# Optimization experiments

Hardware: AMD Instinct MI355X
Metric: run time of the kernel (lower is better)

The kernel has to match this reference:

```python
import jax, jax.numpy as jnp
import numpy as np

B, C, H, W = 4, 16, 512, 512


def setup_inputs() -> dict:
    key = jax.random.key(0)
    k1, k2, k3, k4, k5 = jax.random.split(key, 5)
    # positive depth in [0.5, 10.5] meters
    depth = jax.random.uniform(k1, (B, 1, H, W), dtype=jnp.float32) * 10.0 + 0.5
    # realistic, well-conditioned camera intrinsics per batch element
    fx = 500.0 + 20.0 * jax.random.normal(k2, (B,), dtype=jnp.float32)
    fy = 500.0 + 20.0 * jax.random.normal(k3, (B,), dtype=jnp.float32)
    zeros = jnp.zeros((B,), jnp.float32)
    ones = jnp.ones((B,), jnp.float32)
    K = jnp.stack([
        jnp.stack([fx, zeros, ones * (W / 2.0)], axis=-1),
        jnp.stack([zeros, fy, ones * (H / 2.0)], axis=-1),
        jnp.stack([zeros, zeros, ones], axis=-1),
    ], axis=1)  # [B,3,3]
    # near-identity rigid-ish transforms so homogeneous w ~ 1
    T = jnp.eye(4, dtype=jnp.float32)[None, None] + 0.05 * jax.random.normal(k4, (B, C, 4, 4), dtype=jnp.float32)
    masks = jax.random.randint(k5, (B, C, H, W), 0, 2).astype(jnp.bool_)
    return {"depth": depth, "K": K, "T": T, "masks": masks}


def reference(depth, K, T, masks):
    b, _, h, w = depth.shape
    c = masks.shape[1]
    n = h * w
    eps = 1e-10
    # --- depth -> point cloud ---
    u = jnp.arange(w, dtype=depth.dtype)
    v = jnp.arange(h, dtype=depth.dtype)
    uu, vv = jnp.meshgrid(u, v, indexing='xy')            # [H,W]
    uv1 = jnp.stack([uu, vv, jnp.ones_like(uu)], axis=-1)  # [H,W,3]
    K_inv = jnp.linalg.inv(K)                              # [B,3,3]
    d = jnp.transpose(depth, (0, 2, 3, 1))                 # [B,H,W,1]
    points_3d = jnp.einsum('bij,hwj->bhwi', K_inv, uv1) * d  # [B,H,W,3]
    # --- per-object masked transform (vectorized over all channels) ---
    pts = points_3d.reshape(b, n, 3)
    pts_h = jnp.concatenate([pts, jnp.ones((b, n, 1), pts.dtype)], axis=-1)  # [B,N,4]
    trans_h = jnp.einsum('bcij,bnj->bcni', T, pts_h)       # [B,C,N,4]
    trans3 = trans_h[..., :3] / (trans_h[..., 3:] + eps)   # [B,C,N,3]
    masks_flat = masks.reshape(b, c, n)
    out = pts
    for ci in range(c):
        out = jnp.where(masks_flat[:, ci, :, None], trans3[:, ci], out)
    tp = out.reshape(b, h, w, 3)                           # transformed points
    # --- reproject to depth map (scatter) ---
    p2h = jnp.einsum('bij,bhwj->bhwi', K, tp)              # [B,H,W,3]
    p2 = p2h[..., :2] / (p2h[..., 2:] + eps)
    Z = tp[..., 2]                                         # [B,H,W]
    u_idx = jnp.clip(p2[..., 0], 0, w - 1).astype(jnp.int32)
    v_idx = jnp.clip(p2[..., 1], 0, h - 1).astype(jnp.int32)
    b_idx = jnp.broadcast_to(jnp.arange(b)[:, None, None], (b, h, w))
    depth_map = depth.at[b_idx, 0, v_idx, u_idx].set(Z)
    return depth_map
```

## Files before the change

kernel.cpp:

```cpp
#include <hip/hip_runtime.h>
#include <stdint.h>

constexpr int B = 4, C = 16, H = 512, W = 512;
constexpr int N = H * W;
constexpr int PPT = 4;
constexpr int BLOCK = 256;
constexpr int CHUNK = BLOCK * PPT;
constexpr int BLK_PER_BATCH = N / CHUNK;
constexpr float EPS = 1e-10f;


__global__ __launch_bounds__(256) void project_store_kernel(
    const float* __restrict__ depth,
    const float* __restrict__ K,
    const float* __restrict__ T,
    const int*   __restrict__ masks,
    unsigned long long* __restrict__ keys,
    unsigned long long* __restrict__ recs)
{
    __shared__ float Ts[16][17];

    int b = blockIdx.x >> 8;
    int base = (blockIdx.x & (BLK_PER_BATCH - 1)) * CHUNK;
    int n0 = base + threadIdx.x * PPT;
    int idx0 = b * N + n0;
    int vrow = n0 >> 9;
    int u0 = n0 & (W - 1);

    {
        int t = threadIdx.x;
        int c = t >> 4, e = t & 15;
        Ts[e][c] = T[(size_t)b * 256 + t];
    }
    __syncthreads();

    float4 d4 = *(const float4*)(depth + idx0);
    float darr[PPT] = {d4.x, d4.y, d4.z, d4.w};

    const float* Kb = K + b * 9;
    float k00 = Kb[0], k01 = Kb[1], k02 = Kb[2];
    float k10 = Kb[3], k11 = Kb[4], k12 = Kb[5];
    float k20 = Kb[6], k21 = Kb[7], k22 = Kb[8];

    float c00 =  (k11 * k22 - k12 * k21);
    float c01 = -(k10 * k22 - k12 * k20);
    float c02 =  (k10 * k21 - k11 * k20);
    float det = k00 * c00 + k01 * c01 + k02 * c02;
    float invdet = 1.0f / det;
    float i00 =  (k11 * k22 - k12 * k21) * invdet;
    float i01 = -(k01 * k22 - k02 * k21) * invdet;
    float i02 =  (k01 * k12 - k02 * k11) * invdet;
    float i10 = -(k10 * k22 - k12 * k20) * invdet;
    float i11 =  (k00 * k22 - k02 * k20) * invdet;
    float i12 = -(k00 * k12 - k02 * k10) * invdet;
    float i20 =  (k10 * k21 - k11 * k20) * invdet;
    float i21 = -(k00 * k21 - k01 * k20) * invdet;
    float i22 =  (k00 * k11 - k01 * k10) * invdet;

    float vf = (float)vrow;
    float rx = i01 * vf + i02;
    float ry = i11 * vf + i12;
    float rz = i21 * vf + i22;

    const int* mb = masks + (size_t)b * C * N + n0;
    int sel[PPT] = {-1, -1, -1, -1};
    {
        int4 m3 = *(const int4*)(mb + (size_t)15 * N);
        int4 m2 = *(const int4*)(mb + (size_t)14 * N);
        int4 m1 = *(const int4*)(mb + (size_t)13 * N);
        int4 m0 = *(const int4*)(mb + (size_t)12 * N);
        int a3[4] = {m3.x, m3.y, m3.z, m3.w};
        int a2[4] = {m2.x, m2.y, m2.z, m2.w};
        int a1[4] = {m1.x, m1.y, m1.z, m1.w};
        int a0[4] = {m0.x, m0.y, m0.z, m0.w};
        #pragma unroll
        for (int j = 0; j < PPT; ++j)
            sel[j] = a3[j] ? 15 : a2[j] ? 14 : a1[j] ? 13 : a0[j] ? 12 : -1;
        #pragma unroll
        for (int tier = 2; tier >= 0; --tier) {
            if (sel[0] < 0 || sel[1] < 0 || sel[2] < 0 || sel[3] < 0) {
                int cbase = tier * 4;
                int4 q3 = *(const int4*)(mb + (size_t)(cbase + 3) * N);
                int4 q2 = *(const int4*)(mb + (size_t)(cbase + 2) * N);
                int4 q1 = *(const int4*)(mb + (size_t)(cbase + 1) * N);
                int4 q0 = *(const int4*)(mb + (size_t)(cbase + 0) * N);
                int b3[4] = {q3.x, q3.y, q3.z, q3.w};
                int b2[4] = {q2.x, q2.y, q2.z, q2.w};
                int b1[4] = {q1.x, q1.y, q1.z, q1.w};
                int b0[4] = {q0.x, q0.y, q0.z, q0.w};
                #pragma unroll
                for (int j = 0; j < PPT; ++j)
                    if (sel[j] < 0)
                        sel[j] = b3[j] ? cbase + 3 : b2[j] ? cbase + 2
                               : b1[j] ? cbase + 1 : b0[j] ? cbase : -1;
            }
        }
    }

    unsigned long long rec[PPT];
    #pragma unroll
    for (int j = 0; j < PPT; ++j) {
        float d = darr[j];
        float uf = (float)(u0 + j);
        float px = (i00 * uf + rx) * d;
        float py = (i10 * uf + ry) * d;
        float pz = (i20 * uf + rz) * d;

        float ox = px, oy = py, oz = pz;
        int s = sel[j];
        if (s >= 0) {
            float tx = Ts[0][s]  * px + Ts[1][s]  * py + Ts[2][s]  * pz + Ts[3][s];
            float ty = Ts[4][s]  * px + Ts[5][s]  * py + Ts[6][s]  * pz + Ts[7][s];
            float tz = Ts[8][s]  * px + Ts[9][s]  * py + Ts[10][s] * pz + Ts[11][s];
            float tw = Ts[12][s] * px + Ts[13][s] * py + Ts[14][s] * pz + Ts[15][s];
            float denom = tw + EPS;
            ox = tx / denom;
            oy = ty / denom;
            oz = tz / denom;
        }

        float qx = k00 * ox + k01 * oy + k02 * oz;
        float qy = k10 * ox + k11 * oy + k12 * oz;
        float qz = k20 * ox + k21 * oy + k22 * oz;
        float zz = qz + EPS;
        float pu = qx / zz;
        float pv = qy / zz;
        pu = fminf(fmaxf(pu, 0.0f), (float)(W - 1));
        pv = fminf(fmaxf(pv, 0.0f), (float)(H - 1));
        int ui = (int)pu;
        int vi = (int)pv;
        unsigned t = (unsigned)(vi * W + ui);
        unsigned zbits = __float_as_uint(oz);

        rec[j] = ((unsigned long long)t << 32) | (unsigned long long)zbits;
        keys[(size_t)b * N + t] =
            ((unsigned long long)(unsigned)(n0 + j) << 32)
            | (unsigned long long)zbits;
    }

    ulonglong2* rp = (ulonglong2*)(recs + idx0);
    rp[0] = make_ulonglong2(rec[0], rec[1]);
    rp[1] = make_ulonglong2(rec[2], rec[3]);
}

__global__ __launch_bounds__(256) void fixup_kernel(
    unsigned long long* __restrict__ keys,
    const unsigned long long* __restrict__ recs)
{
    __shared__ unsigned slot[CHUNK];

    int b = blockIdx.x >> 8;
    int base = (blockIdx.x & (BLK_PER_BATCH - 1)) * CHUNK;
    int l0 = threadIdx.x * PPT;
    int idx0 = b * N + base + l0;

    #pragma unroll
    for (int j = 0; j < PPT; ++j) slot[threadIdx.x + j * BLOCK] = 0;
    __syncthreads();

    const ulonglong2* rp = (const ulonglong2*)(recs + idx0);
    ulonglong2 r01 = rp[0];
    ulonglong2 r23 = rp[1];
    unsigned long long rec[PPT] = {r01.x, r01.y, r23.x, r23.y};
    unsigned t[PPT], z[PPT];
    #pragma unroll
    for (int j = 0; j < PPT; ++j) {
        t[j] = (unsigned)(rec[j] >> 32);
        z[j] = (unsigned)rec[j];
        atomicMax(&slot[t[j] & (CHUNK - 1)],
                  (t[j] << 10) | (unsigned)(l0 + j));
    }
    __syncthreads();

    #pragma unroll
    for (int j = 0; j < PPT; ++j) {
        unsigned l = (unsigned)(l0 + j);
        unsigned v = slot[t[j] & (CHUNK - 1)];
        if ((v >> 10) == t[j] && (v & (CHUNK - 1)) > l) continue;
        unsigned n = (unsigned)base + l;
        unsigned long long* cell = &keys[(size_t)b * N + t[j]];
        unsigned hi = (unsigned)(*cell >> 32);
        if (hi > (unsigned)(N - 1) || hi < n) {
            unsigned long long key =
                ((unsigned long long)n << 32) | (unsigned long long)z[j];
            atomicMax(cell, key);
        }
    }
}

__global__ __launch_bounds__(256) void resolve_kernel(
    const unsigned long long* __restrict__ keys,
    const float*              __restrict__ depth,
    float*                    __restrict__ out)
{
    int idx0 = (blockIdx.x * BLOCK + threadIdx.x) * PPT;
    const ulonglong2* kp = (const ulonglong2*)(keys + idx0);
    ulonglong2 k01 = kp[0];
    ulonglong2 k23 = kp[1];
    unsigned long long k[PPT] = {k01.x, k01.y, k23.x, k23.y};
    float4 d4 = *(const float4*)(depth + idx0);
    float darr[PPT] = {d4.x, d4.y, d4.z, d4.w};
    float o[PPT];
    #pragma unroll
    for (int j = 0; j < PPT; ++j) {
        unsigned hi = (unsigned)(k[j] >> 32);
        o[j] = (hi <= (unsigned)(N - 1)) ? __uint_as_float((unsigned)k[j])
                                         : darr[j];
    }
    *(float4*)(out + idx0) = make_float4(o[0], o[1], o[2], o[3]);
}

extern "C" void kernel_launch(void* const* d_in, const int* in_sizes, int n_in,
                              void* d_out, int out_size, void* d_ws, size_t ws_size,
                              hipStream_t stream) {
    const float* depth = (const float*)d_in[0];
    const float* K     = (const float*)d_in[1];
    const float* T     = (const float*)d_in[2];
    const int*   masks = (const int*)d_in[3];
    float* out = (float*)d_out;

    char* ws = (char*)d_ws;
    unsigned long long* keys = (unsigned long long*)ws;
    unsigned long long* recs = (unsigned long long*)(ws + (size_t)B * N * 8);

    int grid = B * BLK_PER_BATCH;
    project_store_kernel<<<grid, BLOCK, 0, stream>>>(depth, K, T, masks, keys, recs);
    fixup_kernel<<<grid, BLOCK, 0, stream>>>(keys, recs);
    resolve_kernel<<<grid, BLOCK, 0, stream>>>(keys, depth, out);
}
```

Baseline: 135.1 us.

## Fuse project, fixup and resolve into one cooperative kernel with grid syncs

Merges the three kernels into a single cooperative launch that separates the phases with grid-wide syncs. Projected target indices and depths stay in registers instead of going through a recs buffer, and depth is reused from registers in the resolve phase. This removes two launches and the recs write and read. In exchange it adds two grid-wide barriers and requires all 1024 blocks to be co-resident, hence the launch_bounds occupancy hint of 4 blocks per SM. The Ts array is aliased onto the slot shared buffer.

New measurement: 364.3 us. +169.7%, slower.

```diff
diff --git a/kernel.cpp b/kernel.cpp
--- a/kernel.cpp
+++ b/kernel.cpp
@@ -1,5 +1,8 @@
 #include <hip/hip_runtime.h>
+#include <hip/hip_cooperative_groups.h>
 #include <stdint.h>
+
+namespace cg = cooperative_groups;
 
 constexpr int B = 4, C = 16, H = 512, W = 512;
 constexpr int N = H * W;
@@ -10,15 +13,18 @@
 constexpr float EPS = 1e-10f;
 
 
-__global__ __launch_bounds__(256) void project_store_kernel(
+__global__ __launch_bounds__(BLOCK, 4) void fused_kernel(
     const float* __restrict__ depth,
     const float* __restrict__ K,
     const float* __restrict__ T,
     const int*   __restrict__ masks,
     unsigned long long* __restrict__ keys,
-    unsigned long long* __restrict__ recs)
+    float* __restrict__ out)
 {
-    __shared__ float Ts[16][17];
+    cg::grid_group grid = cg::this_grid();
+
+    __shared__ unsigned sh_slot[CHUNK];
+    float (*Ts)[17] = (float(*)[17])sh_slot;
 
     int b = blockIdx.x >> 8;
     int base = (blockIdx.x & (BLK_PER_BATCH - 1)) * CHUNK;
@@ -97,7 +103,7 @@
         }
     }
 
-    unsigned long long rec[PPT];
+    unsigned tArr[PPT], zArr[PPT];
     #pragma unroll
     for (int j = 0; j < PPT; ++j) {
         float d = darr[j];
@@ -129,82 +135,53 @@
         pv = fminf(fmaxf(pv, 0.0f), (float)(H - 1));
         int ui = (int)pu;
         int vi = (int)pv;
-        unsigned t = (unsigned)(vi * W + ui);
-        unsigned zbits = __float_as_uint(oz);
-
-        rec[j] = ((unsigned long long)t << 32) | (unsigned long long)zbits;
-        keys[(size_t)b * N + t] =
+        tArr[j] = (unsigned)(vi * W + ui);
+        zArr[j] = __float_as_uint(oz);
+
+        keys[(size_t)b * N + tArr[j]] =
             ((unsigned long long)(unsigned)(n0 + j) << 32)
-            | (unsigned long long)zbits;
-    }
-
-    ulonglong2* rp = (ulonglong2*)(recs + idx0);
-    rp[0] = make_ulonglong2(rec[0], rec[1]);
-    rp[1] = make_ulonglong2(rec[2], rec[3]);
-}
-
-__global__ __launch_bounds__(256) void fixup_kernel(
-    unsigned long long* __restrict__ keys,
-    const unsigned long long* __restrict__ recs)
-{
-    __shared__ unsigned slot[CHUNK];
-
-    int b = blockIdx.x >> 8;
-    int base = (blockIdx.x & (BLK_PER_BATCH - 1)) * CHUNK;
+            | (unsigned long long)zArr[j];
+    }
+
+    grid.sync();
+
+    #pragma unroll
+    for (int j = 0; j < PPT; ++j) sh_slot[threadIdx.x + j * BLOCK] = 0;
+    __syncthreads();
+
     int l0 = threadIdx.x * PPT;
-    int idx0 = b * N + base + l0;
-
-    #pragma unroll
-    for (int j = 0; j < PPT; ++j) slot[threadIdx.x + j * BLOCK] = 0;
-    __syncthreads();
-
-    const ulonglong2* rp = (const ulonglong2*)(recs + idx0);
-    ulonglong2 r01 = rp[0];
-    ulonglong2 r23 = rp[1];
-    unsigned long long rec[PPT] = {r01.x, r01.y, r23.x, r23.y};
-    unsigned t[PPT], z[PPT];
-    #pragma unroll
-    for (int j = 0; j < PPT; ++j) {
-        t[j] = (unsigned)(rec[j] >> 32);
-        z[j] = (unsigned)rec[j];
-        atomicMax(&slot[t[j] & (CHUNK - 1)],
-                  (t[j] << 10) | (unsigned)(l0 + j));
-    }
+    #pragma unroll
+    for (int j = 0; j < PPT; ++j)
+        atomicMax(&sh_slot[tArr[j] & (CHUNK - 1)],
+                  (tArr[j] << 10) | (unsigned)(l0 + j));
     __syncthreads();
 
     #pragma unroll
     for (int j = 0; j < PPT; ++j) {
         unsigned l = (unsigned)(l0 + j);
-        unsigned v = slot[t[j] & (CHUNK - 1)];
-        if ((v >> 10) == t[j] && (v & (CHUNK - 1)) > l) continue;
+        unsigned v = sh_slot[tArr[j] & (CHUNK - 1)];
+        if ((v >> 10) == tArr[j] && (v & (CHUNK - 1)) > l) continue;
         unsigned n = (unsigned)base + l;
-        unsigned long long* cell = &keys[(size_t)b * N + t[j]];
+        unsigned long long* cell = &keys[(size_t)b * N + tArr[j]];
         unsigned hi = (unsigned)(*cell >> 32);
         if (hi > (unsigned)(N - 1) || hi < n) {
             unsigned long long key =
-                ((unsigned long long)n << 32) | (unsigned long long)z[j];
+                ((unsigned long long)n << 32) | (unsigned long long)zArr[j];
             atomicMax(cell, key);
         }
     }
-}
-
-__global__ __launch_bounds__(256) void resolve_kernel(
-    const unsigned long long* __restrict__ keys,
-    const float*              __restrict__ depth,
-    float*                    __restrict__ out)
-{
-    int idx0 = (blockIdx.x * BLOCK + threadIdx.x) * PPT;
+
+    grid.sync();
+
     const ulonglong2* kp = (const ulonglong2*)(keys + idx0);
-    ulonglong2 k01 = kp[0];
-    ulonglong2 k23 = kp[1];
-    unsigned long long k[PPT] = {k01.x, k01.y, k23.x, k23.y};
-    float4 d4 = *(const float4*)(depth + idx0);
-    float darr[PPT] = {d4.x, d4.y, d4.z, d4.w};
+    ulonglong2 k01v = kp[0];
+    ulonglong2 k23v = kp[1];
+    unsigned long long kk[PPT] = {k01v.x, k01v.y, k23v.x, k23v.y};
     float o[PPT];
     #pragma unroll
     for (int j = 0; j < PPT; ++j) {
-        unsigned hi = (unsigned)(k[j] >> 32);
-        o[j] = (hi <= (unsigned)(N - 1)) ? __uint_as_float((unsigned)k[j])
+        unsigned hi = (unsigned)(kk[j] >> 32);
+        o[j] = (hi <= (unsigned)(N - 1)) ? __uint_as_float((unsigned)kk[j])
                                          : darr[j];
     }
     *(float4*)(out + idx0) = make_float4(o[0], o[1], o[2], o[3]);
@@ -219,12 +196,11 @@
     const int*   masks = (const int*)d_in[3];
     float* out = (float*)d_out;
 
-    char* ws = (char*)d_ws;
-    unsigned long long* keys = (unsigned long long*)ws;
-    unsigned long long* recs = (unsigned long long*)(ws + (size_t)B * N * 8);
-
-    int grid = B * BLK_PER_BATCH;
-    project_store_kernel<<<grid, BLOCK, 0, stream>>>(depth, K, T, masks, keys, recs);
-    fixup_kernel<<<grid, BLOCK, 0, stream>>>(keys, recs);
-    resolve_kernel<<<grid, BLOCK, 0, stream>>>(keys, depth, out);
+    unsigned long long* keys = (unsigned long long*)d_ws;
+
+    void* args[] = {(void*)&depth, (void*)&K, (void*)&T, (void*)&masks,
+                    (void*)&keys, (void*)&out};
+    hipLaunchCooperativeKernel((void*)fused_kernel,
+                               dim3(B * BLK_PER_BATCH), dim3(BLOCK),
+                               args, 0, stream);
 }
```
